# Optimization experiments

Measured on AMD Instinct MI355X. Metric: run time of the kernel, lower is better.

The kernel has to match this reference:

```python
import jax, jax.numpy as jnp
import numpy as np

B, W, K = 8, 200, 100   # batch, window_size, n_features
KS = 7                   # conv kernel size
HID = 150                # GRU hidden dim
ALPHA = 0.2              # leaky relu slope
FE = 2 * W               # feature GAT embed dim (gatv2 doubles window_size)
TE = 2 * K               # temporal GAT embed dim (gatv2 doubles n_features)


def setup_inputs() -> dict:
    key = jax.random.key(0)
    ks = jax.random.split(key, 16)
    s = lambda k, shape, sc=0.05: jax.random.normal(k, shape, jnp.float32) * sc
    return {
        "x": jax.random.normal(ks[0], (B, W, K), jnp.float32),
        "conv_w": s(ks[1], (K, K, KS)),
        "conv_b": s(ks[2], (K,)),
        "f_lin_w": s(ks[3], (2 * W, FE)),
        "f_lin_b": s(ks[4], (FE,)),
        "f_a": s(ks[5], (FE,)),
        "f_bias": s(ks[6], (K, K)),
        "t_lin_w": s(ks[7], (2 * K, TE)),
        "t_lin_b": s(ks[8], (TE,)),
        "t_a": s(ks[9], (TE,)),
        "t_bias": s(ks[10], (W, W)),
        "w_ih": s(ks[11], (3 * HID, 3 * K)),
        "w_hh": s(ks[12], (3 * HID, HID)),
        "b_ih": s(ks[13], (3 * HID,)),
        "b_hh": s(ks[14], (3 * HID,)),
    }


def _leaky(x):
    return jnp.where(x >= 0, x, ALPHA * x)


def _gatv2(v, lin_w, lin_b, a, bias):
    """GATv2 layer over fully-connected graph. v: (b, N, D).
    e_ij = a . leakyrelu(W [v_i || v_j] + b_lin); out = sigmoid(softmax(e+bias) @ v).
    Splitting W rows avoids materializing the (b,N,N,2D) concat tensor."""
    D = v.shape[-1]
    w1, w2 = lin_w[:D], lin_w[D:]
    si = jnp.einsum('bnd,de->bne', v, w1)  # contribution of node i (repeated)
    sj = jnp.einsum('bnd,de->bne', v, w2)  # contribution of node j (alternating)
    g = _leaky(si[:, :, None, :] + sj[:, None, :, :] + lin_b)  # (b,N,N,E)
    e = jnp.einsum('bije,e->bij', g, a) + bias                 # (b,N,N)
    attn = jax.nn.softmax(e, axis=2)
    return jax.nn.sigmoid(jnp.einsum('bij,bjd->bid', attn, v))  # (b,N,D)


def _forward(x, conv_w, conv_b, f_lin_w, f_lin_b, f_a, f_bias,
             t_lin_w, t_lin_b, t_a, t_bias, w_ih, w_hh, b_ih, b_hh):
    # ConvLayer: permute to (b,K,W), pad 3 both sides, conv1d k=7, relu, permute back
    xc = jnp.transpose(x, (0, 2, 1))
    xc = jax.lax.conv_general_dilated(xc, conv_w, (1,), [((KS - 1) // 2, (KS - 1) // 2)],
                                      dimension_numbers=('NCH', 'OIH', 'NCH'))
    xc = jax.nn.relu(xc + conv_b[None, :, None])
    xc = jnp.transpose(xc, (0, 2, 1))  # (b, W, K)

    # Feature GAT: nodes = features, per-node vector = window
    h_feat = _gatv2(jnp.transpose(xc, (0, 2, 1)), f_lin_w, f_lin_b, f_a, f_bias)
    h_feat = jnp.transpose(h_feat, (0, 2, 1))  # (b, W, K)
    # Temporal GAT: nodes = timesteps, per-node vector = features
    h_temp = _gatv2(xc, t_lin_w, t_lin_b, t_a, t_bias)  # (b, W, K)

    h_cat = jnp.concatenate([xc, h_feat, h_temp], axis=2)  # (b, W, 3K)

    # Single-layer GRU, torch gate order (r, z, n), batch_first; return final hidden
    def step(h, xt):
        gi = xt @ w_ih.T + b_ih
        gh = h @ w_hh.T + b_hh
        ir, iz, inn = jnp.split(gi, 3, axis=-1)
        hr, hz, hn = jnp.split(gh, 3, axis=-1)
        r = jax.nn.sigmoid(ir + hr)
        z = jax.nn.sigmoid(iz + hz)
        n = jnp.tanh(inn + r * hn)
        return (1.0 - z) * n + z * h, None

    h0 = jnp.zeros((x.shape[0], HID), x.dtype)
    h_end, _ = jax.lax.scan(step, h0, jnp.transpose(h_cat, (1, 0, 2)))
    return h_end  # (b, HID)


def reference(x, conv_w, conv_b, f_lin_w, f_lin_b, f_a, f_bias,
              t_lin_w, t_lin_b, t_a, t_bias, w_ih, w_hh, b_ih, b_hh):
    return _forward(x, conv_w, conv_b, f_lin_w, f_lin_b, f_a, f_bias,
                    t_lin_w, t_lin_b, t_a, t_bias, w_ih, w_hh, b_ih, b_hh)
```

## Files before the change

kernel.cpp:

```cpp
#include <hip/hip_runtime.h>
#include <math.h>

#define NB   8
#define NW   200
#define NK   100
#define KSZ  7
#define NHID 150
#define NFE  400
#define NTE  200
#define NG   450
#define NCIN 300
#define ALPHAC 0.2f

typedef __attribute__((ext_vector_type(8))) short bf8;
typedef __attribute__((ext_vector_type(4))) float f32x4;

__device__ __forceinline__ float sigmoidf_(float x){
  return 1.0f/(1.0f + __expf(-x));
}
__device__ __forceinline__ float tanhf_(float x){
  float xc = fminf(fmaxf(x, -15.f), 15.f);
  float e = __expf(2.f*xc);
  return (e - 1.f)/(e + 1.f);
}
__device__ __forceinline__ unsigned short f2bf(float f){
  unsigned int u = __float_as_uint(f);
  unsigned int r = u + 0x7FFFu + ((u>>16)&1u);
  return (unsigned short)(r>>16);
}

__global__ void prep_kernel(const float* conv_w, const float* w_ih, const float* w_hh,
                            float* conv_wT, float* w_ihT, unsigned int* Bfrag){
  int idx = blockIdx.x*256 + threadIdx.x;
  const int n1 = NK*NK*KSZ;
  const int n2 = NG*NCIN;
  const int n3 = 32*5*64*4;
  if (idx < n1){
    int k = idx % NK; int it = idx / NK;
    int i = it / KSZ, t = it % KSZ;
    conv_wT[idx] = conv_w[(k*NK + i)*KSZ + t];
  } else if (idx < n1 + n2){
    int o = idx - n1; int g = o % NG; int c = o / NG;
    w_ihT[o] = w_ih[g*NCIN + c];
  } else if (idx < n1 + n2 + n3){
    int o = idx - n1 - n2;
    int n   = o / 1280;
    int rem = o % 1280;
    int ks  = rem / 256;
    int rem2= rem % 256;
    int l   = rem2 >> 2;
    int d   = rem2 & 3;
    int col = n*16 + (l & 15);
    int k0  = ks*32 + (l >> 4)*8 + d*2;
    unsigned short lo = 0, hi = 0;
    if (col < NG){
      if (k0     < NHID) lo = f2bf(w_hh[col*NHID + k0]);
      if (k0 + 1 < NHID) hi = f2bf(w_hh[col*NHID + k0 + 1]);
    }
    Bfrag[o] = ((unsigned int)hi << 16) | lo;
  }
}

__global__ void conv_kernel(const float* x, const float* conv_b, const float* conv_wT, float* xc){
  int idx = blockIdx.x*256 + threadIdx.x;
  if (idx >= NB*NW*NK) return;
  int k = idx % NK; int w = (idx/NK) % NW; int b = idx/(NK*NW);
  float acc = conv_b[k];
  const float* xb = x + b*NW*NK;
  for (int t = 0; t < KSZ; ++t){
    int ws = w + t - 3;
    if (ws < 0 || ws >= NW) continue;
    const float* xr = xb + ws*NK;
    const float* wr = conv_wT + t*NK + k;
    #pragma unroll 4
    for (int i = 0; i < NK; ++i){
      acc += xr[i] * wr[i*KSZ*NK];
    }
  }
  xc[idx] = fmaxf(acc, 0.0f);
}

__global__ void fgat_sisj(const float* xc, const float* f_lin_w, float* si, float* sj){
  __shared__ __align__(16) float vt[NW*4];
  int b = blockIdx.x / 25; int n0 = (blockIdx.x % 25)*4;
  int tid = threadIdx.x;
  for (int idx = tid; idx < NW*4; idx += 512){
    int d = idx >> 2, nn = idx & 3;
    vt[idx] = xc[(b*NW + d)*NK + n0 + nn];
  }
  __syncthreads();
  if (tid >= NFE) return;
  int e = tid;
  float a1[4] = {0,0,0,0}, a2[4] = {0,0,0,0};
  for (int d = 0; d < NW; ++d){
    float w1 = f_lin_w[d*NFE + e];
    float w2 = f_lin_w[(NW + d)*NFE + e];
    float4 v = *(const float4*)&vt[d*4];
    a1[0] += v.x*w1; a1[1] += v.y*w1; a1[2] += v.z*w1; a1[3] += v.w*w1;
    a2[0] += v.x*w2; a2[1] += v.y*w2; a2[2] += v.z*w2; a2[3] += v.w*w2;
  }
  #pragma unroll
  for (int nn = 0; nn < 4; ++nn){
    si[(b*NK + n0+nn)*NFE + e] = a1[nn];
    sj[(b*NK + n0+nn)*NFE + e] = a2[nn];
  }
}

__global__ void tgat_sisj(const float* xc, const float* t_lin_w, float* si, float* sj){
  __shared__ __align__(16) float vt[NK*4];
  int b = blockIdx.x / 50; int n0 = (blockIdx.x % 50)*4;
  int tid = threadIdx.x;
  for (int idx = tid; idx < NK*4; idx += 256){
    int d = idx >> 2, nn = idx & 3;
    vt[idx] = xc[(b*NW + n0+nn)*NK + d];
  }
  __syncthreads();
  if (tid >= NTE) return;
  int e = tid;
  float a1[4] = {0,0,0,0}, a2[4] = {0,0,0,0};
  for (int d = 0; d < NK; ++d){
    float w1 = t_lin_w[d*NTE + e];
    float w2 = t_lin_w[(NK + d)*NTE + e];
    float4 v = *(const float4*)&vt[d*4];
    a1[0] += v.x*w1; a1[1] += v.y*w1; a1[2] += v.z*w1; a1[3] += v.w*w1;
    a2[0] += v.x*w2; a2[1] += v.y*w2; a2[2] += v.z*w2; a2[3] += v.w*w2;
  }
  #pragma unroll
  for (int nn = 0; nn < 4; ++nn){
    si[(b*NW + n0+nn)*NTE + e] = a1[nn];
    sj[(b*NW + n0+nn)*NTE + e] = a2[nn];
  }
}

__global__ void fgat_attn(const float* xc, const float* si, const float* sj,
                          const float* f_lin_b, const float* f_a, const float* f_bias,
                          float* h_featT){
  __shared__ float sib[NFE], av[NFE], attn[NK], red[128];
  int b = blockIdx.x / NK, i = blockIdx.x % NK;
  int tid = threadIdx.x;
  for (int e = tid; e < NFE; e += 128){
    sib[e] = si[(b*NK + i)*NFE + e] + f_lin_b[e];
    av[e]  = f_a[e];
  }
  __syncthreads();
  float ej = -1e30f;
  if (tid < NK){
    const float* sjr = sj + (b*NK + tid)*NFE;
    float acc = 0.f;
    for (int e = 0; e < NFE; ++e){
      float tv = sib[e] + sjr[e];
      float lk = fmaxf(tv, 0.f) + ALPHAC*fminf(tv, 0.f);
      acc += av[e]*lk;
    }
    ej = acc + f_bias[i*NK + tid];
  }
  red[tid] = ej; __syncthreads();
  for (int s = 64; s > 0; s >>= 1){ if (tid < s) red[tid] = fmaxf(red[tid], red[tid+s]); __syncthreads(); }
  float m = red[0]; __syncthreads();
  float ex = (tid < NK) ? __expf(ej - m) : 0.f;
  red[tid] = ex; __syncthreads();
  for (int s = 64; s > 0; s >>= 1){ if (tid < s) red[tid] += red[tid+s]; __syncthreads(); }
  float denom = red[0];
  if (tid < NK) attn[tid] = ex / denom;
  __syncthreads();
  for (int d = tid; d < NW; d += 128){
    const float* xr = xc + (b*NW + d)*NK;
    float acc = 0.f;
    for (int j = 0; j < NK; ++j) acc += attn[j]*xr[j];
    h_featT[(b*NW + d)*NK + i] = sigmoidf_(acc);
  }
}

__global__ void tgat_attn(const float* xc, const float* si, const float* sj,
                          const float* t_lin_b, const float* t_a, const float* t_bias,
                          float* h_temp){
  __shared__ float sib[NTE], av[NTE], attn[NW], red[256];
  int b = blockIdx.x / NW, i = blockIdx.x % NW;
  int tid = threadIdx.x;
  for (int e = tid; e < NTE; e += 256){
    sib[e] = si[(b*NW + i)*NTE + e] + t_lin_b[e];
    av[e]  = t_a[e];
  }
  __syncthreads();
  float ej = -1e30f;
  if (tid < NW){
    const float* sjr = sj + (b*NW + tid)*NTE;
    float acc = 0.f;
    for (int e = 0; e < NTE; ++e){
      float tv = sib[e] + sjr[e];
      float lk = fmaxf(tv, 0.f) + ALPHAC*fminf(tv, 0.f);
      acc += av[e]*lk;
    }
    ej = acc + t_bias[i*NW + tid];
  }
  red[tid] = ej; __syncthreads();
  for (int s = 128; s > 0; s >>= 1){ if (tid < s) red[tid] = fmaxf(red[tid], red[tid+s]); __syncthreads(); }
  float m = red[0]; __syncthreads();
  float ex = (tid < NW) ? __expf(ej - m) : 0.f;
  red[tid] = ex; __syncthreads();
  for (int s = 128; s > 0; s >>= 1){ if (tid < s) red[tid] += red[tid+s]; __syncthreads(); }
  float denom = red[0];
  if (tid < NW) attn[tid] = ex / denom;
  __syncthreads();
  for (int d = tid; d < NK; d += 256){
    float acc = 0.f;
    for (int j = 0; j < NW; ++j) acc += attn[j]*xc[(b*NW + j)*NK + d];
    h_temp[(b*NW + i)*NK + d] = sigmoidf_(acc);
  }
}

__global__ void gi_kernel(const float* xc, const float* h_featT, const float* h_temp,
                          const float* w_ihT, const float* b_ih, float* gi){
  __shared__ __align__(16) float hc[NCIN*8];
  int b = blockIdx.x / 25; int t0 = (blockIdx.x % 25)*8;
  int tid = threadIdx.x;
  for (int idx = tid; idx < NCIN*8; idx += 512){
    int tt = idx / NCIN; int c = idx % NCIN;
    int base = (b*NW + t0 + tt)*NK;
    float v;
    if (c < NK)        v = xc[base + c];
    else if (c < 2*NK) v = h_featT[base + c - NK];
    else               v = h_temp[base + c - 2*NK];
    hc[c*8 + tt] = v;
  }
  __syncthreads();
  if (tid >= NG) return;
  int g = tid;
  float bi = b_ih[g];
  float acc[8];
  #pragma unroll
  for (int tt = 0; tt < 8; ++tt) acc[tt] = bi;
  for (int c = 0; c < NCIN; ++c){
    float wv = w_ihT[c*NG + g];
    float4 h0 = *(const float4*)&hc[c*8];
    float4 h1 = *(const float4*)&hc[c*8+4];
    acc[0] += h0.x*wv; acc[1] += h0.y*wv; acc[2] += h0.z*wv; acc[3] += h0.w*wv;
    acc[4] += h1.x*wv; acc[5] += h1.y*wv; acc[6] += h1.z*wv; acc[7] += h1.w*wv;
  }
  #pragma unroll
  for (int tt = 0; tt < 8; ++tt)
    gi[((t0+tt)*NB + b)*NG + g] = acc[tt];
}

#define MM(C, A, Bf) C = __builtin_amdgcn_mfma_f32_16x16x32_bf16(A, Bf, C, 0, 0, 0);
#define TILE_MM(C, K0,K1,K2,K3,K4) \
  MM(C,aH0,K0) MM(C,aL0,K0) MM(C,aH1,K1) MM(C,aL1,K1) MM(C,aH2,K2) MM(C,aL2,K2) \
  MM(C,aH3,K3) MM(C,aL3,K3) MM(C,aH4,K4) MM(C,aL4,K4)
#define LDB(NM, TL, KS) bf8 NM = Bfrag[((TL)*5 + (KS))*64 + lane];

__global__ void __launch_bounds__(512, 2) gru_kernel(const float* gi, const bf8* Bfrag,
                                                     const float* b_hh, float* out){
  __shared__ __align__(16) unsigned short h_hi[16*176];
  __shared__ __align__(16) unsigned short h_lo[16*176];
  __shared__ __align__(16) float h_f32[8*152];
  __shared__ __align__(16) float gh[16*516];
  int tid = threadIdx.x;
  int lane = tid & 63;
  int wv = tid >> 6;
  int agrp = lane >> 4;
  int arow = lane & 15;
  int crow = agrp*4;
  int ccol = arow;

  int p0 = tid, p1 = tid + 512, p2 = tid + 1024;
  int b0 = p0/NHID, u0 = p0%NHID;
  int b1 = p1/NHID, u1 = p1%NHID;
  bool v2 = (p2 < NB*NHID);
  int b2 = v2 ? p2/NHID : 0, u2 = v2 ? p2%NHID : 0;
  float bhr0 = b_hh[u0],      bhz0 = b_hh[NHID+u0],  bhn0 = b_hh[2*NHID+u0];
  float bhr1 = b_hh[u1],      bhz1 = b_hh[NHID+u1],  bhn1 = b_hh[2*NHID+u1];
  float bhr2 = b_hh[u2],      bhz2 = b_hh[NHID+u2],  bhn2 = b_hh[2*NHID+u2];

  LDB(W00,wv,0)    LDB(W01,wv,1)    LDB(W02,wv,2)    LDB(W03,wv,3)    LDB(W04,wv,4)
  LDB(W10,wv+8,0)  LDB(W11,wv+8,1)  LDB(W12,wv+8,2)  LDB(W13,wv+8,3)  LDB(W14,wv+8,4)
  LDB(W20,wv+16,0) LDB(W21,wv+16,1) LDB(W22,wv+16,2) LDB(W23,wv+16,3) LDB(W24,wv+16,4)
  LDB(W30,wv+24,0) LDB(W31,wv+24,1) LDB(W32,wv+24,2) LDB(W33,wv+24,3) LDB(W34,wv+24,4)

  for (int i = tid; i < 16*176; i += 512){ h_hi[i] = 0; h_lo[i] = 0; }
  for (int i = tid; i < 8*152;  i += 512){ h_f32[i] = 0.f; }
  __syncthreads();

  const bf8* HH = (const bf8*)h_hi;
  const bf8* HL = (const bf8*)h_lo;
  int abase = arow*22 + agrp;

  for (int t = 0; t < NW; ++t){
    const float* gt = gi + t*NB*NG;
    float gr0 = gt[b0*NG+u0], gz0 = gt[b0*NG+NHID+u0], gn0 = gt[b0*NG+2*NHID+u0];
    float gr1 = gt[b1*NG+u1], gz1 = gt[b1*NG+NHID+u1], gn1 = gt[b1*NG+2*NHID+u1];
    float gr2 = 0.f, gz2 = 0.f, gn2 = 0.f;
    if (v2){ gr2 = gt[b2*NG+u2]; gz2 = gt[b2*NG+NHID+u2]; gn2 = gt[b2*NG+2*NHID+u2]; }

    bf8 aH0 = HH[abase],    aH1 = HH[abase+4],  aH2 = HH[abase+8],
        aH3 = HH[abase+12], aH4 = HH[abase+16];
    bf8 aL0 = HL[abase],    aL1 = HL[abase+4],  aL2 = HL[abase+8],
        aL3 = HL[abase+12], aL4 = HL[abase+16];

    f32x4 c0 = {0.f,0.f,0.f,0.f}, c1 = {0.f,0.f,0.f,0.f},
          c2 = {0.f,0.f,0.f,0.f}, c3 = {0.f,0.f,0.f,0.f};
    TILE_MM(c0, W00,W01,W02,W03,W04)
    TILE_MM(c1, W10,W11,W12,W13,W14)
    TILE_MM(c2, W20,W21,W22,W23,W24)
    TILE_MM(c3, W30,W31,W32,W33,W34)

    if (agrp < 2){
      float* g0 = &gh[crow*516 + (wv   )*16 + ccol];
      float* g1 = &gh[crow*516 + (wv+ 8)*16 + ccol];
      float* g2 = &gh[crow*516 + (wv+16)*16 + ccol];
      float* g3 = &gh[crow*516 + (wv+24)*16 + ccol];
      g0[0]=c0[0]; g0[516]=c0[1]; g0[1032]=c0[2]; g0[1548]=c0[3];
      g1[0]=c1[0]; g1[516]=c1[1]; g1[1032]=c1[2]; g1[1548]=c1[3];
      g2[0]=c2[0]; g2[516]=c2[1]; g2[1032]=c2[2]; g2[1548]=c2[3];
      g3[0]=c3[0]; g3[516]=c3[1]; g3[1032]=c3[2]; g3[1548]=c3[3];
    }
    __syncthreads();

    {
      float r = sigmoidf_(gr0 + gh[b0*516+u0] + bhr0);
      float z = sigmoidf_(gz0 + gh[b0*516+NHID+u0] + bhz0);
      float n = tanhf_  (gn0 + r*(gh[b0*516+2*NHID+u0] + bhn0));
      float hold = h_f32[b0*152+u0];
      float hn = (1.f - z)*n + z*hold;
      h_f32[b0*152+u0] = hn;
      unsigned int ub = __float_as_uint(hn);
      unsigned int hi = (ub + 0x7FFFu + ((ub>>16)&1u)) >> 16;
      h_hi[b0*176+u0] = (unsigned short)hi;
      float lo = hn - __uint_as_float(hi<<16);
      unsigned int ul = __float_as_uint(lo);
      h_lo[b0*176+u0] = (unsigned short)((ul + 0x7FFFu + ((ul>>16)&1u)) >> 16);
    }
    {
      float r = sigmoidf_(gr1 + gh[b1*516+u1] + bhr1);
      float z = sigmoidf_(gz1 + gh[b1*516+NHID+u1] + bhz1);
      float n = tanhf_  (gn1 + r*(gh[b1*516+2*NHID+u1] + bhn1));
      float hold = h_f32[b1*152+u1];
      float hn = (1.f - z)*n + z*hold;
      h_f32[b1*152+u1] = hn;
      unsigned int ub = __float_as_uint(hn);
      unsigned int hi = (ub + 0x7FFFu + ((ub>>16)&1u)) >> 16;
      h_hi[b1*176+u1] = (unsigned short)hi;
      float lo = hn - __uint_as_float(hi<<16);
      unsigned int ul = __float_as_uint(lo);
      h_lo[b1*176+u1] = (unsigned short)((ul + 0x7FFFu + ((ul>>16)&1u)) >> 16);
    }
    if (v2){
      float r = sigmoidf_(gr2 + gh[b2*516+u2] + bhr2);
      float z = sigmoidf_(gz2 + gh[b2*516+NHID+u2] + bhz2);
      float n = tanhf_  (gn2 + r*(gh[b2*516+2*NHID+u2] + bhn2));
      float hold = h_f32[b2*152+u2];
      float hn = (1.f - z)*n + z*hold;
      h_f32[b2*152+u2] = hn;
      unsigned int ub = __float_as_uint(hn);
      unsigned int hi = (ub + 0x7FFFu + ((ub>>16)&1u)) >> 16;
      h_hi[b2*176+u2] = (unsigned short)hi;
      float lo = hn - __uint_as_float(hi<<16);
      unsigned int ul = __float_as_uint(lo);
      h_lo[b2*176+u2] = (unsigned short)((ul + 0x7FFFu + ((ul>>16)&1u)) >> 16);
    }
    __syncthreads();
  }

  out[b0*NHID + u0] = h_f32[b0*152 + u0];
  out[b1*NHID + u1] = h_f32[b1*152 + u1];
  if (v2) out[b2*NHID + u2] = h_f32[b2*152 + u2];
}

extern "C" void kernel_launch(void* const* d_in, const int* in_sizes, int n_in,
                              void* d_out, int out_size, void* d_ws, size_t ws_size,
                              hipStream_t stream){
  const float* x       = (const float*)d_in[0];
  const float* conv_w  = (const float*)d_in[1];
  const float* conv_b  = (const float*)d_in[2];
  const float* f_lin_w = (const float*)d_in[3];
  const float* f_lin_b = (const float*)d_in[4];
  const float* f_a     = (const float*)d_in[5];
  const float* f_bias  = (const float*)d_in[6];
  const float* t_lin_w = (const float*)d_in[7];
  const float* t_lin_b = (const float*)d_in[8];
  const float* t_a     = (const float*)d_in[9];
  const float* t_bias  = (const float*)d_in[10];
  const float* w_ih    = (const float*)d_in[11];
  const float* w_hh    = (const float*)d_in[12];
  const float* b_ih    = (const float*)d_in[13];
  const float* b_hh    = (const float*)d_in[14];

  float* ws      = (float*)d_ws;
  float* xc      = ws;
  float* conv_wT = ws + 160000;
  float* si_f    = ws + 230000;
  float* sj_f    = ws + 550000;
  float* h_featT = ws + 870000;
  float* si_t    = ws + 1030000;
  float* sj_t    = ws + 1350000;
  float* h_temp  = ws + 1670000;
  float* w_ihT   = ws + 1830000;
  float* gi      = ws + 1965000;
  float* BfragF  = ws + 2685000;

  prep_kernel<<<961, 256, 0, stream>>>(conv_w, w_ih, w_hh, conv_wT, w_ihT, (unsigned int*)BfragF);
  conv_kernel<<<(NB*NW*NK + 255)/256, 256, 0, stream>>>(x, conv_b, conv_wT, xc);
  fgat_sisj<<<NB*25, 512, 0, stream>>>(xc, f_lin_w, si_f, sj_f);
  tgat_sisj<<<NB*50, 256, 0, stream>>>(xc, t_lin_w, si_t, sj_t);
  fgat_attn<<<NB*NK, 128, 0, stream>>>(xc, si_f, sj_f, f_lin_b, f_a, f_bias, h_featT);
  tgat_attn<<<NB*NW, 256, 0, stream>>>(xc, si_t, sj_t, t_lin_b, t_a, t_bias, h_temp);
  gi_kernel<<<NB*25, 512, 0, stream>>>(xc, h_featT, h_temp, w_ihT, b_ih, gi);
  gru_kernel<<<1, 512, 0, stream>>>(gi, (const bf8*)BfragF, b_hh, (float*)d_out);
}
```

Before: 478.1 us.

## Pack hi/lo bf16 hidden state into one MFMA tile, keep weights in AGPRs

The GRU recurrence previously issued two MFMAs per K-slice, one for the hi and one for the lo bf16 part of the hidden state, using only 8 of the 16 A-matrix rows. The hi parts now go in rows 0-7 and the lo parts in rows 8-15 of a single bf16 buffer, so each K-slice needs one MFMA, and the two partial rows are summed in the gate computation. The recurrent weight fragments are pinned in AGPRs through inline asm with manual s_nop hazard padding, to free VGPRs and shorten the serial per-step MFMA chain. The hand-written asm carries a risk of hazard or register-allocation errors, and the extra shared-memory reads per gate add a small cost.

```diff
diff --git a/kernel.cpp b/kernel.cpp
--- a/kernel.cpp
+++ b/kernel.cpp
@@ -242,16 +242,24 @@
     gi[((t0+tt)*NB + b)*NG + g] = acc[tt];
 }
 
-#define MM(C, A, Bf) C = __builtin_amdgcn_mfma_f32_16x16x32_bf16(A, Bf, C, 0, 0, 0);
-#define TILE_MM(C, K0,K1,K2,K3,K4) \
-  MM(C,aH0,K0) MM(C,aL0,K0) MM(C,aH1,K1) MM(C,aL1,K1) MM(C,aH2,K2) MM(C,aL2,K2) \
-  MM(C,aH3,K3) MM(C,aL3,K3) MM(C,aH4,K4) MM(C,aL4,K4)
-#define LDB(NM, TL, KS) bf8 NM = Bfrag[((TL)*5 + (KS))*64 + lane];
-
-__global__ void __launch_bounds__(512, 2) gru_kernel(const float* gi, const bf8* Bfrag,
+#define STASH(B0,B1,B2,B3, FR) { \
+  int4 wq = Bq[(FR)*64 + lane]; \
+  asm volatile("v_accvgpr_write_b32 " B0 ", %0\n\t" \
+               "v_accvgpr_write_b32 " B1 ", %1\n\t" \
+               "v_accvgpr_write_b32 " B2 ", %2\n\t" \
+               "v_accvgpr_write_b32 " B3 ", %3" \
+               :: "v"(wq.x), "v"(wq.y), "v"(wq.z), "v"(wq.w) \
+               : B0, B1, B2, B3); }
+#define MMA_INIT(ACC, AF, BR, C0,C1,C2,C3) \
+  asm volatile("v_mfma_f32_16x16x32_bf16 %0, %1, " BR ", 0" \
+               : "=v"(ACC) : "v"(AF) : C0,C1,C2,C3);
+#define MMA_ACC(ACC, AF, BR, C0,C1,C2,C3) \
+  asm volatile("v_mfma_f32_16x16x32_bf16 %0, %1, " BR ", %0" \
+               : "+v"(ACC) : "v"(AF) : C0,C1,C2,C3);
+
+__global__ void __launch_bounds__(512, 2) gru_kernel(const float* gi, const int4* Bq,
                                                      const float* b_hh, float* out){
-  __shared__ __align__(16) unsigned short h_hi[16*176];
-  __shared__ __align__(16) unsigned short h_lo[16*176];
+  __shared__ __align__(16) unsigned short h_bf[16*176];
   __shared__ __align__(16) float h_f32[8*152];
   __shared__ __align__(16) float gh[16*516];
   int tid = threadIdx.x;
@@ -267,21 +275,36 @@
   int b1 = p1/NHID, u1 = p1%NHID;
   bool v2 = (p2 < NB*NHID);
   int b2 = v2 ? p2/NHID : 0, u2 = v2 ? p2%NHID : 0;
-  float bhr0 = b_hh[u0],      bhz0 = b_hh[NHID+u0],  bhn0 = b_hh[2*NHID+u0];
-  float bhr1 = b_hh[u1],      bhz1 = b_hh[NHID+u1],  bhn1 = b_hh[2*NHID+u1];
-  float bhr2 = b_hh[u2],      bhz2 = b_hh[NHID+u2],  bhn2 = b_hh[2*NHID+u2];
-
-  LDB(W00,wv,0)    LDB(W01,wv,1)    LDB(W02,wv,2)    LDB(W03,wv,3)    LDB(W04,wv,4)
-  LDB(W10,wv+8,0)  LDB(W11,wv+8,1)  LDB(W12,wv+8,2)  LDB(W13,wv+8,3)  LDB(W14,wv+8,4)
-  LDB(W20,wv+16,0) LDB(W21,wv+16,1) LDB(W22,wv+16,2) LDB(W23,wv+16,3) LDB(W24,wv+16,4)
-  LDB(W30,wv+24,0) LDB(W31,wv+24,1) LDB(W32,wv+24,2) LDB(W33,wv+24,3) LDB(W34,wv+24,4)
-
-  for (int i = tid; i < 16*176; i += 512){ h_hi[i] = 0; h_lo[i] = 0; }
-  for (int i = tid; i < 8*152;  i += 512){ h_f32[i] = 0.f; }
-  __syncthreads();
-
-  const bf8* HH = (const bf8*)h_hi;
-  const bf8* HL = (const bf8*)h_lo;
+  float bhr0 = b_hh[u0], bhz0 = b_hh[NHID+u0], bhn0 = b_hh[2*NHID+u0];
+  float bhr1 = b_hh[u1], bhz1 = b_hh[NHID+u1], bhn1 = b_hh[2*NHID+u1];
+  float bhr2 = b_hh[u2], bhz2 = b_hh[NHID+u2], bhn2 = b_hh[2*NHID+u2];
+
+  STASH("a0","a1","a2","a3",     (wv)*5+0)
+  STASH("a4","a5","a6","a7",     (wv)*5+1)
+  STASH("a8","a9","a10","a11",   (wv)*5+2)
+  STASH("a12","a13","a14","a15", (wv)*5+3)
+  STASH("a16","a17","a18","a19", (wv)*5+4)
+  STASH("a20","a21","a22","a23", (wv+8)*5+0)
+  STASH("a24","a25","a26","a27", (wv+8)*5+1)
+  STASH("a28","a29","a30","a31", (wv+8)*5+2)
+  STASH("a32","a33","a34","a35", (wv+8)*5+3)
+  STASH("a36","a37","a38","a39", (wv+8)*5+4)
+  STASH("a40","a41","a42","a43", (wv+16)*5+0)
+  STASH("a44","a45","a46","a47", (wv+16)*5+1)
+  STASH("a48","a49","a50","a51", (wv+16)*5+2)
+  STASH("a52","a53","a54","a55", (wv+16)*5+3)
+  STASH("a56","a57","a58","a59", (wv+16)*5+4)
+  STASH("a60","a61","a62","a63", (wv+24)*5+0)
+  STASH("a64","a65","a66","a67", (wv+24)*5+1)
+  STASH("a68","a69","a70","a71", (wv+24)*5+2)
+  STASH("a72","a73","a74","a75", (wv+24)*5+3)
+  STASH("a76","a77","a78","a79", (wv+24)*5+4)
+
+  for (int i = tid; i < 16*176; i += 512) h_bf[i] = 0;
+  for (int i = tid; i < 8*152;  i += 512) h_f32[i] = 0.f;
+  __syncthreads();
+
+  const bf8* HB = (const bf8*)h_bf;
   int abase = arow*22 + agrp;
 
   for (int t = 0; t < NW; ++t){
@@ -291,19 +314,33 @@
     float gr2 = 0.f, gz2 = 0.f, gn2 = 0.f;
     if (v2){ gr2 = gt[b2*NG+u2]; gz2 = gt[b2*NG+NHID+u2]; gn2 = gt[b2*NG+2*NHID+u2]; }
 
-    bf8 aH0 = HH[abase],    aH1 = HH[abase+4],  aH2 = HH[abase+8],
-        aH3 = HH[abase+12], aH4 = HH[abase+16];
-    bf8 aL0 = HL[abase],    aL1 = HL[abase+4],  aL2 = HL[abase+8],
-        aL3 = HL[abase+12], aL4 = HL[abase+16];
-
-    f32x4 c0 = {0.f,0.f,0.f,0.f}, c1 = {0.f,0.f,0.f,0.f},
-          c2 = {0.f,0.f,0.f,0.f}, c3 = {0.f,0.f,0.f,0.f};
-    TILE_MM(c0, W00,W01,W02,W03,W04)
-    TILE_MM(c1, W10,W11,W12,W13,W14)
-    TILE_MM(c2, W20,W21,W22,W23,W24)
-    TILE_MM(c3, W30,W31,W32,W33,W34)
-
-    if (agrp < 2){
+    bf8 A0 = HB[abase],    A1 = HB[abase+4],  A2 = HB[abase+8],
+        A3 = HB[abase+12], A4 = HB[abase+16];
+
+    f32x4 c0, c1, c2, c3;
+    MMA_INIT(c0, A0, "a[0:3]",   "a0","a1","a2","a3")
+    MMA_INIT(c1, A0, "a[20:23]", "a20","a21","a22","a23")
+    MMA_INIT(c2, A0, "a[40:43]", "a40","a41","a42","a43")
+    MMA_INIT(c3, A0, "a[60:63]", "a60","a61","a62","a63")
+    MMA_ACC (c0, A1, "a[4:7]",   "a4","a5","a6","a7")
+    MMA_ACC (c1, A1, "a[24:27]", "a24","a25","a26","a27")
+    MMA_ACC (c2, A1, "a[44:47]", "a44","a45","a46","a47")
+    MMA_ACC (c3, A1, "a[64:67]", "a64","a65","a66","a67")
+    MMA_ACC (c0, A2, "a[8:11]",  "a8","a9","a10","a11")
+    MMA_ACC (c1, A2, "a[28:31]", "a28","a29","a30","a31")
+    MMA_ACC (c2, A2, "a[48:51]", "a48","a49","a50","a51")
+    MMA_ACC (c3, A2, "a[68:71]", "a68","a69","a70","a71")
+    MMA_ACC (c0, A3, "a[12:15]", "a12","a13","a14","a15")
+    MMA_ACC (c1, A3, "a[32:35]", "a32","a33","a34","a35")
+    MMA_ACC (c2, A3, "a[52:55]", "a52","a53","a54","a55")
+    MMA_ACC (c3, A3, "a[72:75]", "a72","a73","a74","a75")
+    MMA_ACC (c0, A4, "a[16:19]", "a16","a17","a18","a19")
+    MMA_ACC (c1, A4, "a[36:39]", "a36","a37","a38","a39")
+    MMA_ACC (c2, A4, "a[56:59]", "a56","a57","a58","a59")
+    MMA_ACC (c3, A4, "a[76:79]", "a76","a77","a78","a79")
+    asm volatile("s_nop 7\n\ts_nop 7" ::: );
+
+    {
       float* g0 = &gh[crow*516 + (wv   )*16 + ccol];
       float* g1 = &gh[crow*516 + (wv+ 8)*16 + ccol];
       float* g2 = &gh[crow*516 + (wv+16)*16 + ccol];
@@ -316,46 +353,46 @@
     __syncthreads();
 
     {
-      float r = sigmoidf_(gr0 + gh[b0*516+u0] + bhr0);
-      float z = sigmoidf_(gz0 + gh[b0*516+NHID+u0] + bhz0);
-      float n = tanhf_  (gn0 + r*(gh[b0*516+2*NHID+u0] + bhn0));
+      float r = sigmoidf_(gr0 + gh[b0*516+u0]        + gh[(8+b0)*516+u0]        + bhr0);
+      float z = sigmoidf_(gz0 + gh[b0*516+NHID+u0]   + gh[(8+b0)*516+NHID+u0]   + bhz0);
+      float n = tanhf_  (gn0 + r*(gh[b0*516+2*NHID+u0] + gh[(8+b0)*516+2*NHID+u0] + bhn0));
       float hold = h_f32[b0*152+u0];
       float hn = (1.f - z)*n + z*hold;
       h_f32[b0*152+u0] = hn;
       unsigned int ub = __float_as_uint(hn);
       unsigned int hi = (ub + 0x7FFFu + ((ub>>16)&1u)) >> 16;
-      h_hi[b0*176+u0] = (unsigned short)hi;
+      h_bf[b0*176+u0] = (unsigned short)hi;
       float lo = hn - __uint_as_float(hi<<16);
       unsigned int ul = __float_as_uint(lo);
-      h_lo[b0*176+u0] = (unsigned short)((ul + 0x7FFFu + ((ul>>16)&1u)) >> 16);
+      h_bf[(8+b0)*176+u0] = (unsigned short)((ul + 0x7FFFu + ((ul>>16)&1u)) >> 16);
     }
     {
-      float r = sigmoidf_(gr1 + gh[b1*516+u1] + bhr1);
-      float z = sigmoidf_(gz1 + gh[b1*516+NHID+u1] + bhz1);
-      float n = tanhf_  (gn1 + r*(gh[b1*516+2*NHID+u1] + bhn1));
+      float r = sigmoidf_(gr1 + gh[b1*516+u1]        + gh[(8+b1)*516+u1]        + bhr1);
+      float z = sigmoidf_(gz1 + gh[b1*516+NHID+u1]   + gh[(8+b1)*516+NHID+u1]   + bhz1);
+      float n = tanhf_  (gn1 + r*(gh[b1*516+2*NHID+u1] + gh[(8+b1)*516+2*NHID+u1] + bhn1));
       float hold = h_f32[b1*152+u1];
       float hn = (1.f - z)*n + z*hold;
       h_f32[b1*152+u1] = hn;
       unsigned int ub = __float_as_uint(hn);
       unsigned int hi = (ub + 0x7FFFu + ((ub>>16)&1u)) >> 16;
-      h_hi[b1*176+u1] = (unsigned short)hi;
+      h_bf[b1*176+u1] = (unsigned short)hi;
       float lo = hn - __uint_as_float(hi<<16);
       unsigned int ul = __float_as_uint(lo);
-      h_lo[b1*176+u1] = (unsigned short)((ul + 0x7FFFu + ((ul>>16)&1u)) >> 16);
+      h_bf[(8+b1)*176+u1] = (unsigned short)((ul + 0x7FFFu + ((ul>>16)&1u)) >> 16);
     }
     if (v2){
-      float r = sigmoidf_(gr2 + gh[b2*516+u2] + bhr2);
-      float z = sigmoidf_(gz2 + gh[b2*516+NHID+u2] + bhz2);
-      float n = tanhf_  (gn2 + r*(gh[b2*516+2*NHID+u2] + bhn2));
+      float r = sigmoidf_(gr2 + gh[b2*516+u2]        + gh[(8+b2)*516+u2]        + bhr2);
+      float z = sigmoidf_(gz2 + gh[b2*516+NHID+u2]   + gh[(8+b2)*516+NHID+u2]   + bhz2);
+      float n = tanhf_  (gn2 + r*(gh[b2*516+2*NHID+u2] + gh[(8+b2)*516+2*NHID+u2] + bhn2));
       float hold = h_f32[b2*152+u2];
       float hn = (1.f - z)*n + z*hold;
       h_f32[b2*152+u2] = hn;
       unsigned int ub = __float_as_uint(hn);
       unsigned int hi = (ub + 0x7FFFu + ((ub>>16)&1u)) >> 16;
-      h_hi[b2*176+u2] = (unsigned short)hi;
+      h_bf[b2*176+u2] = (unsigned short)hi;
       float lo = hn - __uint_as_float(hi<<16);
       unsigned int ul = __float_as_uint(lo);
-      h_lo[b2*176+u2] = (unsigned short)((ul + 0x7FFFu + ((ul>>16)&1u)) >> 16);
+      h_bf[(8+b2)*176+u2] = (unsigned short)((ul + 0x7FFFu + ((ul>>16)&1u)) >> 16);
     }
     __syncthreads();
   }
@@ -404,5 +441,5 @@
   fgat_attn<<<NB*NK, 128, 0, stream>>>(xc, si_f, sj_f, f_lin_b, f_a, f_bias, h_featT);
   tgat_attn<<<NB*NW, 256, 0, stream>>>(xc, si_t, sj_t, t_lin_b, t_a, t_bias, h_temp);
   gi_kernel<<<NB*25, 512, 0, stream>>>(xc, h_featT, h_temp, w_ihT, b_ih, gi);
-  gru_kernel<<<1, 512, 0, stream>>>(gi, (const bf8*)BfragF, b_hh, (float*)d_out);
-}
+  gru_kernel<<<1, 512, 0, stream>>>(gi, (const int4*)BfragF, b_hh, (float*)d_out);
+}
```

After: 434.7 us. 9.1% less time.
